# Kernel optimization log

Measured on AMD Instinct MI355X. Metric: run time of the kernel, lower is better.

Reference implementation:

```python
import jax, jax.numpy as jnp
import numpy as np

D_MODEL = 1024
D_STATE = 16
D_CONV = 4
EXPAND = 2
D_INNER = EXPAND * D_MODEL          # 2048
DT_RANK = (D_MODEL + 15) // 16      # 64
BATCH = 1
SEQLEN = 1024


def setup_inputs() -> dict:
    key = jax.random.key(0)
    ks = jax.random.split(key, 9)
    s = 0.02  # weight scale for numerical stability
    x = jax.random.normal(ks[0], (BATCH, SEQLEN, D_MODEL), jnp.float32)
    W_in = jax.random.normal(ks[1], (2 * D_INNER, D_MODEL), jnp.float32) * s
    conv_w = jax.random.normal(ks[2], (D_INNER, D_CONV), jnp.float32) * 0.1
    conv_b = jax.random.normal(ks[3], (D_INNER,), jnp.float32) * 0.1
    W_xproj = jax.random.normal(ks[4], (DT_RANK + 2 * D_STATE, D_INNER), jnp.float32) * s
    W_dt = jax.random.normal(ks[5], (D_INNER, DT_RANK), jnp.float32) * s
    b_dt = jax.random.normal(ks[6], (D_INNER,), jnp.float32) * 0.1
    # official init: A = repeat(arange(1, d_state+1), 'n -> d n'); A_log = log(A)
    A_log = jnp.log(jnp.tile(jnp.arange(1, D_STATE + 1, dtype=jnp.float32), (D_INNER, 1)))
    D_skip = jnp.ones((D_INNER,), jnp.float32)
    W_out = jax.random.normal(ks[7], (D_MODEL, D_INNER), jnp.float32) * s
    return {"x": x, "W_in": W_in, "conv_w": conv_w, "conv_b": conv_b,
            "W_xproj": W_xproj, "W_dt": W_dt, "b_dt": b_dt,
            "A_log": A_log, "D_skip": D_skip, "W_out": W_out}


def _mamba_fwd(x, W_in, conv_w, conv_b, W_xproj, W_dt, b_dt, A_log, D_skip, W_out):
    B, L, _ = x.shape
    # input projection -> (B, L, 2*d_inner), split into x-branch and gate z
    xz = x @ W_in.T
    xi, z = jnp.split(xz, 2, axis=-1)
    # causal depthwise conv1d over length
    xc = jnp.transpose(xi, (0, 2, 1))  # (B, d_inner, L)
    xc = jax.lax.conv_general_dilated(
        xc, conv_w[:, None, :], window_strides=(1,),
        padding=[(D_CONV - 1, 0)], feature_group_count=D_INNER)
    xc = jax.nn.silu(xc + conv_b[None, :, None])
    xi = jnp.transpose(xc, (0, 2, 1))  # (B, L, d_inner)
    # data-dependent SSM parameters
    x_dbl = xi @ W_xproj.T  # (B, L, dt_rank + 2*d_state)
    dt, Bm, Cm = jnp.split(x_dbl, [DT_RANK, DT_RANK + D_STATE], axis=-1)
    delta = jax.nn.softplus(dt @ W_dt.T + b_dt)  # (B, L, d_inner)
    A = -jnp.exp(A_log)  # (d_inner, d_state)
    # discretize: h_t = exp(delta*A) * h_{t-1} + (delta*x) * B_t
    deltaA = jnp.exp(jnp.einsum('bld,dn->bldn', delta, A))          # (B,L,d,n)
    deltaBx = jnp.einsum('bld,bln->bldn', delta * xi, Bm)            # (B,L,d,n)

    def step(h, inp):
        dA_t, dBx_t, c_t = inp
        h = dA_t * h + dBx_t                    # (B, d_inner, d_state)
        y = jnp.einsum('bdn,bn->bd', h, c_t)    # (B, d_inner)
        return h, y

    h0 = jnp.zeros((B, D_INNER, D_STATE), x.dtype)
    _, ys = jax.lax.scan(step, h0, (jnp.transpose(deltaA, (1, 0, 2, 3)),
                                    jnp.transpose(deltaBx, (1, 0, 2, 3)),
                                    jnp.transpose(Cm, (1, 0, 2))))
    y = jnp.transpose(ys, (1, 0, 2))  # (B, L, d_inner)
    y = y + xi * D_skip
    y = y * jax.nn.silu(z)
    return y @ W_out.T  # (B, L, d_model)


def reference(x, W_in, conv_w, conv_b, W_xproj, W_dt, b_dt, A_log, D_skip, W_out):
    return _mamba_fwd(x, W_in, conv_w, conv_b, W_xproj, W_dt, b_dt, A_log, D_skip, W_out)
```

## Files before the change

kernel.cpp:

```cpp
#include <hip/hip_runtime.h>
#include <hip/hip_bf16.h>
#include <math.h>

namespace {

constexpr int SEQ    = 1024;
constexpr int DMODEL = 1024;
constexpr int DINNER = 2048;
constexpr int DSTATE = 16;
constexpr int DTRANK = 64;
constexpr int XPW    = 96;
constexpr int XPWP   = 128;

typedef __attribute__((ext_vector_type(8))) short short8;
typedef __attribute__((ext_vector_type(4))) short short4_t;
typedef __attribute__((ext_vector_type(4))) float floatx4;

#define GLB __attribute__((address_space(1)))
#define LDSAS __attribute__((address_space(3)))

__device__ __forceinline__ float siluf(float x) { return x / (1.f + __expf(-x)); }

__device__ __forceinline__ unsigned short f2b(float f) {
    __hip_bfloat16 h = __float2bfloat16(f);
    return *reinterpret_cast<unsigned short*>(&h);
}
__device__ __forceinline__ float b2f(unsigned short u) {
    union { unsigned int i; float f; } v; v.i = (unsigned int)u << 16; return v.f;
}

constexpr size_t N_XB   = (size_t)SEQ * DMODEL;
constexpr size_t N_WIN  = (size_t)2 * DINNER * DMODEL;
constexpr size_t N_WXP  = (size_t)XPWP * DINNER;
constexpr size_t N_WDT  = (size_t)DINNER * DTRANK;
constexpr size_t N_WOUT = (size_t)DMODEL * DINNER;
constexpr size_t CO1 = N_XB, CO2 = CO1 + N_WIN, CO3 = CO2 + N_WXP,
                 CO4 = CO3 + N_WDT, CO5 = CO4 + N_WOUT;

__global__ __launch_bounds__(256)
void cast_all(const float* __restrict__ x, const float* __restrict__ Win,
              const float* __restrict__ Wxp, const float* __restrict__ Wdt,
              const float* __restrict__ Wout, unsigned short* __restrict__ dst)
{
    size_t i = ((size_t)blockIdx.x * 256 + threadIdx.x) * 8;
    if (i >= CO5) return;
    const float* src; size_t si;
    if (i < CO1)      { src = x;   si = i; }
    else if (i < CO2) { src = Win; si = i - CO1; }
    else if (i < CO3) {
        size_t j = i - CO2, row = j / DINNER;
        if (row >= XPW) { short8 z = {0,0,0,0,0,0,0,0};
                          *reinterpret_cast<short8*>(&dst[i]) = z; return; }
        src = Wxp; si = j;
    }
    else if (i < CO4) { src = Wdt;  si = i - CO3; }
    else              { src = Wout; si = i - CO4; }
    float4 a = *reinterpret_cast<const float4*>(&src[si]);
    float4 b = *reinterpret_cast<const float4*>(&src[si + 4]);
    short8 o;
    o[0]=(short)f2b(a.x); o[1]=(short)f2b(a.y); o[2]=(short)f2b(a.z); o[3]=(short)f2b(a.w);
    o[4]=(short)f2b(b.x); o[5]=(short)f2b(b.y); o[6]=(short)f2b(b.z); o[7]=(short)f2b(b.w);
    *reinterpret_cast<short8*>(&dst[i]) = o;
}

template<int EPI>
__global__ __launch_bounds__(256)
void gemm_mfma(const unsigned short* __restrict__ A, int lda,
               const unsigned short* __restrict__ B, int ldb,
               float* __restrict__ C, int ldc, size_t czstride,
               const float* __restrict__ bias, int Ksub, int nbx)
{
    constexpr int BM = 64, BN = 128, BK = 32, MR = 2, NR = 4;
    __shared__ unsigned short Alds[2][BM * BK];
    __shared__ unsigned short Blds[2][BN * BK];

    const int nwg = gridDim.x;
    int id = blockIdx.x;
    int wg = ((nwg & 7) == 0) ? (id & 7) * (nwg >> 3) + (id >> 3) : id;
    const int bx = wg % nbx, by = wg / nbx;

    const int tid  = threadIdx.x;
    const int lane = tid & 63;
    const int wv   = tid >> 6;
    const int wm   = wv >> 1, wn = wv & 1;
    const int fr   = lane & 15;
    const int kg   = lane >> 4;
    const int m0   = by * BM;
    const int n0   = bx * BN;
    const int kb   = blockIdx.z * Ksub;
    const int srow = tid >> 2;
    const int scol = (tid & 3) * 8;
    float* Cz = C + (size_t)blockIdx.z * czstride;

    floatx4 acc[MR][NR];
#pragma unroll
    for (int mi = 0; mi < MR; ++mi)
#pragma unroll
        for (int ni = 0; ni < NR; ++ni)
            acc[mi][ni] = (floatx4){0.f, 0.f, 0.f, 0.f};

    auto stage = [&](int buf, int k0) {
        __builtin_amdgcn_global_load_lds(
            (const GLB unsigned int*)&A[(size_t)(m0 + srow) * lda + k0 + scol],
            (LDSAS unsigned int*)&Alds[buf][tid * 8], 16, 0, 0);
#pragma unroll
        for (int r = 0; r < 2; ++r)
            __builtin_amdgcn_global_load_lds(
                (const GLB unsigned int*)&B[(size_t)(n0 + r * 64 + srow) * ldb + k0 + scol],
                (LDSAS unsigned int*)&Blds[buf][r * 2048 + tid * 8], 16, 0, 0);
    };

    const int nt = Ksub / BK;
    stage(0, kb);
    __syncthreads();
    int cur = 0;
    for (int t = 0; t < nt; ++t) {
        if (t + 1 < nt) stage(cur ^ 1, kb + (t + 1) * BK);
        short8 af[MR], bf[NR];
#pragma unroll
        for (int mi = 0; mi < MR; ++mi)
            af[mi] = *reinterpret_cast<const short8*>(
                &Alds[cur][(wm * 32 + mi * 16 + fr) * BK + kg * 8]);
#pragma unroll
        for (int ni = 0; ni < NR; ++ni)
            bf[ni] = *reinterpret_cast<const short8*>(
                &Blds[cur][(wn * 64 + ni * 16 + fr) * BK + kg * 8]);
#pragma unroll
        for (int mi = 0; mi < MR; ++mi)
#pragma unroll
            for (int ni = 0; ni < NR; ++ni)
                acc[mi][ni] = __builtin_amdgcn_mfma_f32_16x16x32_bf16(
                    af[mi], bf[ni], acc[mi][ni], 0, 0, 0);
        __syncthreads();
        cur ^= 1;
    }

#pragma unroll
    for (int mi = 0; mi < MR; ++mi)
#pragma unroll
        for (int ni = 0; ni < NR; ++ni)
#pragma unroll
            for (int r = 0; r < 4; ++r) {
                int row = m0 + wm * 32 + mi * 16 + kg * 4 + r;
                int col = n0 + wn * 64 + ni * 16 + fr;
                float v = acc[mi][ni][r];
                if constexpr (EPI == 1) {
                    v += bias[col];
                    v = (v > 20.f) ? v : log1pf(__expf(v));
                }
                Cz[(size_t)row * ldc + col] = v;
            }
}

__global__ __launch_bounds__(256)
void combine_xdbl(const float* __restrict__ xp, float* __restrict__ xf,
                  unsigned short* __restrict__ xb)
{
    int i = (blockIdx.x * 256 + threadIdx.x) * 4;
    constexpr size_t SL = (size_t)SEQ * XPWP;
    float4 s{0.f, 0.f, 0.f, 0.f};
#pragma unroll
    for (int z = 0; z < 8; ++z) {
        float4 p = *reinterpret_cast<const float4*>(&xp[z * SL + i]);
        s.x += p.x; s.y += p.y; s.z += p.z; s.w += p.w;
    }
    *reinterpret_cast<float4*>(&xf[i]) = s;
    short4_t o; o[0]=(short)f2b(s.x); o[1]=(short)f2b(s.y);
                o[2]=(short)f2b(s.z); o[3]=(short)f2b(s.w);
    *reinterpret_cast<short4_t*>(&xb[i]) = o;
}

__global__ __launch_bounds__(256)
void combine_out(const float* __restrict__ op, float* __restrict__ out)
{
    int i = (blockIdx.x * 256 + threadIdx.x) * 4;
    constexpr size_t SL = (size_t)SEQ * DMODEL;
    float4 s0 = *reinterpret_cast<const float4*>(&op[i]);
    float4 s1 = *reinterpret_cast<const float4*>(&op[SL + i]);
    float4 s2 = *reinterpret_cast<const float4*>(&op[2 * SL + i]);
    float4 s3 = *reinterpret_cast<const float4*>(&op[3 * SL + i]);
    float4 s{ s0.x+s1.x+s2.x+s3.x, s0.y+s1.y+s2.y+s3.y,
              s0.z+s1.z+s2.z+s3.z, s0.w+s1.w+s2.w+s3.w };
    *reinterpret_cast<float4*>(&out[i]) = s;
}

__global__ __launch_bounds__(256)
void conv_silu(const float* __restrict__ xz,
               const float* __restrict__ conv_w,
               const float* __restrict__ conv_b,
               unsigned short* __restrict__ xic)
{
    int idx = blockIdx.x * 256 + threadIdx.x;
    int l = idx / DINNER;
    int d = idx % DINNER;
    float acc = conv_b[d];
    float4 w = *reinterpret_cast<const float4*>(&conv_w[d * 4]);
    float wk[4] = {w.x, w.y, w.z, w.w};
#pragma unroll
    for (int k = 0; k < 4; ++k) {
        int ls = l - 3 + k;
        if (ls >= 0) acc = fmaf(xz[(size_t)ls * (2 * DINNER) + d], wk[k], acc);
    }
    xic[idx] = f2b(siluf(acc));
}

__global__ __launch_bounds__(256)
void scan_pass1(const float* __restrict__ delta,
                const unsigned short* __restrict__ xic,
                const float* __restrict__ xdbl,
                const float* __restrict__ A_log,
                float* __restrict__ Pbuf, float* __restrict__ Sbuf, int CH)
{
    const int tid = threadIdx.x;
    const int d   = blockIdx.x * 256 + tid;
    const int c   = blockIdx.y;
    const int tb  = c * CH;

    float An[16], h[16];
#pragma unroll
    for (int n = 0; n < 16; ++n) {
        An[n] = -__expf(A_log[(size_t)d * 16 + n]);
        h[n]  = 0.f;
    }
    float sdl = 0.f;

    __shared__ float Bls[16][16];
    const int sr = tid >> 4, sq = tid & 15;

    for (int s0 = 0; s0 < CH; s0 += 16) {
        Bls[sr][sq] = xdbl[(size_t)(tb + s0 + sr) * XPWP + DTRANK + sq];
        __syncthreads();
#pragma unroll
        for (int tt = 0; tt < 16; ++tt) {
            int t = tb + s0 + tt;
            float dl = delta[(size_t)t * DINNER + d];
            float xv = b2f(xic[(size_t)t * DINNER + d]);
            float t1 = dl * xv;
            sdl += dl;
            floatx4 B0 = *reinterpret_cast<const floatx4*>(&Bls[tt][0]);
            floatx4 B1 = *reinterpret_cast<const floatx4*>(&Bls[tt][4]);
            floatx4 B2 = *reinterpret_cast<const floatx4*>(&Bls[tt][8]);
            floatx4 B3 = *reinterpret_cast<const floatx4*>(&Bls[tt][12]);
#pragma unroll
            for (int n = 0; n < 16; ++n) {
                float bn = (n < 4) ? B0[n] : (n < 8) ? B1[n-4] : (n < 12) ? B2[n-8] : B3[n-12];
                float a  = __expf(dl * An[n]);
                h[n] = fmaf(a, h[n], t1 * bn);
            }
        }
        __syncthreads();
    }
#pragma unroll
    for (int n = 0; n < 16; ++n) {
        size_t o = ((size_t)c * 16 + n) * DINNER + d;
        Pbuf[o] = __expf(sdl * An[n]);
        Sbuf[o] = h[n];
    }
}

__global__ __launch_bounds__(256)
void scan_pass2(const float* __restrict__ Pbuf, float* __restrict__ Sbuf, int NCr)
{
    int idx = blockIdx.x * 256 + threadIdx.x;
    float h = 0.f;
    for (int c = 0; c < NCr; ++c) {
        size_t o = (size_t)c * (DINNER * DSTATE) + idx;
        float p = Pbuf[o], s = Sbuf[o];
        Sbuf[o] = h;
        h = fmaf(p, h, s);
    }
}

__global__ __launch_bounds__(256)
void scan_pass3(const float* __restrict__ delta,
                const unsigned short* __restrict__ xic,
                const float* __restrict__ xdbl,
                const float* __restrict__ A_log,
                const float* __restrict__ D_skip,
                const float* __restrict__ xz,
                const float* __restrict__ Hin,
                unsigned short* __restrict__ yfin, int CH)
{
    const int tid = threadIdx.x;
    const int d   = blockIdx.x * 256 + tid;
    const int c   = blockIdx.y;
    const int tb  = c * CH;

    float An[16], h[16];
#pragma unroll
    for (int n = 0; n < 16; ++n) {
        An[n] = -__expf(A_log[(size_t)d * 16 + n]);
        h[n]  = Hin[((size_t)c * 16 + n) * DINNER + d];
    }
    const float Dsk = D_skip[d];

    __shared__ float Bls[16][32];
    const int sr = tid >> 4, sq = (tid & 15) * 2;

    for (int s0 = 0; s0 < CH; s0 += 16) {
        float2 bc = *reinterpret_cast<const float2*>(
            &xdbl[(size_t)(tb + s0 + sr) * XPWP + DTRANK + sq]);
        Bls[sr][sq] = bc.x; Bls[sr][sq + 1] = bc.y;
        __syncthreads();
#pragma unroll
        for (int tt = 0; tt < 16; ++tt) {
            int t = tb + s0 + tt;
            float dl = delta[(size_t)t * DINNER + d];
            float xv = b2f(xic[(size_t)t * DINNER + d]);
            float zv = xz[(size_t)t * (2 * DINNER) + DINNER + d];
            float t1 = dl * xv;
            floatx4 B0 = *reinterpret_cast<const floatx4*>(&Bls[tt][0]);
            floatx4 B1 = *reinterpret_cast<const floatx4*>(&Bls[tt][4]);
            floatx4 B2 = *reinterpret_cast<const floatx4*>(&Bls[tt][8]);
            floatx4 B3 = *reinterpret_cast<const floatx4*>(&Bls[tt][12]);
            floatx4 C0 = *reinterpret_cast<const floatx4*>(&Bls[tt][16]);
            floatx4 C1 = *reinterpret_cast<const floatx4*>(&Bls[tt][20]);
            floatx4 C2 = *reinterpret_cast<const floatx4*>(&Bls[tt][24]);
            floatx4 C3 = *reinterpret_cast<const floatx4*>(&Bls[tt][28]);
            float y = 0.f;
#pragma unroll
            for (int n = 0; n < 16; ++n) {
                float bn = (n < 4) ? B0[n] : (n < 8) ? B1[n-4] : (n < 12) ? B2[n-8] : B3[n-12];
                float cn = (n < 4) ? C0[n] : (n < 8) ? C1[n-4] : (n < 12) ? C2[n-8] : C3[n-12];
                float a  = __expf(dl * An[n]);
                h[n] = fmaf(a, h[n], t1 * bn);
                y = fmaf(h[n], cn, y);
            }
            float yv = fmaf(xv, Dsk, y) * siluf(zv);
            yfin[(size_t)t * DINNER + d] = f2b(yv);
        }
        __syncthreads();
    }
}

}

extern "C" void kernel_launch(void* const* d_in, const int* in_sizes, int n_in,
                              void* d_out, int out_size, void* d_ws, size_t ws_size,
                              hipStream_t stream)
{
    (void)in_sizes; (void)n_in; (void)out_size;

    const float* x       = (const float*)d_in[0];
    const float* W_in    = (const float*)d_in[1];
    const float* conv_w  = (const float*)d_in[2];
    const float* conv_b  = (const float*)d_in[3];
    const float* W_xproj = (const float*)d_in[4];
    const float* W_dt    = (const float*)d_in[5];
    const float* b_dt    = (const float*)d_in[6];
    const float* A_log   = (const float*)d_in[7];
    const float* D_skip  = (const float*)d_in[8];
    const float* W_out   = (const float*)d_in[9];
    float* out = (float*)d_out;

    const size_t BF16_SHORTS = CO5 + (size_t)SEQ * DINNER + (size_t)SEQ * XPWP
                             + (size_t)SEQ * DINNER;
    const size_t F32_FIXED   = (size_t)SEQ * 2 * DINNER
                             + (size_t)SEQ * DINNER
                             + (size_t)SEQ * XPWP
                             + 8 * (size_t)SEQ * XPWP;
    auto need = [&](int nc) {
        return (F32_FIXED + 2 * (size_t)nc * DINNER * DSTATE) * 4 + BF16_SHORTS * 2;
    };
    int NC = 64;
    if (need(64) > ws_size) NC = 32;
    if (need(32) > ws_size) NC = 16;
    const int CH = SEQ / NC;

    float* ws     = (float*)d_ws;
    float* xz     = ws;
    float* delta  = xz    + (size_t)SEQ * 2 * DINNER;
    float* xdbl_f = delta + (size_t)SEQ * DINNER;
    float* xpart  = xdbl_f + (size_t)SEQ * XPWP;
    float* Pbuf   = xpart + 8 * (size_t)SEQ * XPWP;
    float* Sbuf   = Pbuf  + (size_t)NC * DINNER * DSTATE;
    unsigned short* us     = (unsigned short*)(Sbuf + (size_t)NC * DINNER * DSTATE);
    unsigned short* x_b    = us;
    unsigned short* Win_b  = x_b + CO1;
    unsigned short* Wxp_b  = x_b + CO2;
    unsigned short* Wdt_b  = x_b + CO3;
    unsigned short* Wout_b = x_b + CO4;
    unsigned short* xic_b  = x_b + CO5;
    unsigned short* xdbl_b = xic_b + (size_t)SEQ * DINNER;
    unsigned short* yfin_b = xdbl_b + (size_t)SEQ * XPWP;
    float* opart = xz;

    cast_all<<<(int)((CO5 / 8 + 255) / 256), 256, 0, stream>>>(
        x, W_in, W_xproj, W_dt, W_out, x_b);

    gemm_mfma<0><<<dim3(512, 1, 1), 256, 0, stream>>>(
        x_b, DMODEL, Win_b, DMODEL, xz, 2 * DINNER, 0, nullptr, DMODEL, 32);

    conv_silu<<<(SEQ * DINNER) / 256, 256, 0, stream>>>(xz, conv_w, conv_b, xic_b);

    gemm_mfma<0><<<dim3(16, 1, 8), 256, 0, stream>>>(
        xic_b, DINNER, Wxp_b, DINNER, xpart, XPWP, (size_t)SEQ * XPWP,
        nullptr, DINNER / 8, 1);
    combine_xdbl<<<(SEQ * XPWP) / 1024, 256, 0, stream>>>(xpart, xdbl_f, xdbl_b);

    gemm_mfma<1><<<dim3(256, 1, 1), 256, 0, stream>>>(
        xdbl_b, XPWP, Wdt_b, DTRANK, delta, DINNER, 0, b_dt, DTRANK, 16);

    scan_pass1<<<dim3(DINNER / 256, NC), 256, 0, stream>>>(
        delta, xic_b, xdbl_f, A_log, Pbuf, Sbuf, CH);
    scan_pass2<<<(DINNER * DSTATE) / 256, 256, 0, stream>>>(Pbuf, Sbuf, NC);
    scan_pass3<<<dim3(DINNER / 256, NC), 256, 0, stream>>>(
        delta, xic_b, xdbl_f, A_log, D_skip, xz, Sbuf, yfin_b, CH);

    gemm_mfma<0><<<dim3(128, 1, 4), 256, 0, stream>>>(
        yfin_b, DINNER, Wout_b, DINNER, opart, DMODEL, (size_t)SEQ * DMODEL,
        nullptr, DINNER / 4, 8);
    combine_out<<<(SEQ * DMODEL) / 1024, 256, 0, stream>>>(opart, out);
}
```

Baseline: 136.7 us.

## Shrink GEMM tile to 64x64, fuse silu(z) bf16 epilogue, halve out-proj split-K

Reduces the GEMM tile from 64x128 to 64x64 and doubles grid sizes for all projections. The input-projection epilogue now writes the x-branch in fp32 and the gate as bf16 silu(z), which removes the fp32 z buffer and the silu from the scan. The output projection drops from 4-way to 2-way split-K, so the combine step reads less. Smaller tiles give more workgroups but less data reuse per block, and storing the gate in bf16 adds a little rounding error.

```diff
diff --git a/kernel.cpp b/kernel.cpp
--- a/kernel.cpp
+++ b/kernel.cpp
@@ -68,9 +68,10 @@
 void gemm_mfma(const unsigned short* __restrict__ A, int lda,
                const unsigned short* __restrict__ B, int ldb,
                float* __restrict__ C, int ldc, size_t czstride,
-               const float* __restrict__ bias, int Ksub, int nbx)
-{
-    constexpr int BM = 64, BN = 128, BK = 32, MR = 2, NR = 4;
+               const float* __restrict__ bias, int Ksub, int nbx,
+               unsigned short* __restrict__ gz)
+{
+    constexpr int BM = 64, BN = 64, BK = 32, MR = 2, NR = 2;
     __shared__ unsigned short Alds[2][BM * BK];
     __shared__ unsigned short Blds[2][BN * BK];
 
@@ -103,11 +104,9 @@
         __builtin_amdgcn_global_load_lds(
             (const GLB unsigned int*)&A[(size_t)(m0 + srow) * lda + k0 + scol],
             (LDSAS unsigned int*)&Alds[buf][tid * 8], 16, 0, 0);
-#pragma unroll
-        for (int r = 0; r < 2; ++r)
-            __builtin_amdgcn_global_load_lds(
-                (const GLB unsigned int*)&B[(size_t)(n0 + r * 64 + srow) * ldb + k0 + scol],
-                (LDSAS unsigned int*)&Blds[buf][r * 2048 + tid * 8], 16, 0, 0);
+        __builtin_amdgcn_global_load_lds(
+            (const GLB unsigned int*)&B[(size_t)(n0 + srow) * ldb + k0 + scol],
+            (LDSAS unsigned int*)&Blds[buf][tid * 8], 16, 0, 0);
     };
 
     const int nt = Ksub / BK;
@@ -124,7 +123,7 @@
 #pragma unroll
         for (int ni = 0; ni < NR; ++ni)
             bf[ni] = *reinterpret_cast<const short8*>(
-                &Blds[cur][(wn * 64 + ni * 16 + fr) * BK + kg * 8]);
+                &Blds[cur][(wn * 32 + ni * 16 + fr) * BK + kg * 8]);
 #pragma unroll
         for (int mi = 0; mi < MR; ++mi)
 #pragma unroll
@@ -142,13 +141,20 @@
 #pragma unroll
             for (int r = 0; r < 4; ++r) {
                 int row = m0 + wm * 32 + mi * 16 + kg * 4 + r;
-                int col = n0 + wn * 64 + ni * 16 + fr;
+                int col = n0 + wn * 32 + ni * 16 + fr;
                 float v = acc[mi][ni][r];
                 if constexpr (EPI == 1) {
                     v += bias[col];
                     v = (v > 20.f) ? v : log1pf(__expf(v));
+                    Cz[(size_t)row * ldc + col] = v;
+                } else if constexpr (EPI == 3) {
+                    if (col < DINNER)
+                        Cz[(size_t)row * ldc + col] = v;
+                    else
+                        gz[(size_t)row * DINNER + col - DINNER] = f2b(siluf(v));
+                } else {
+                    Cz[(size_t)row * ldc + col] = v;
                 }
-                Cz[(size_t)row * ldc + col] = v;
             }
 }
 
@@ -177,15 +183,12 @@
     constexpr size_t SL = (size_t)SEQ * DMODEL;
     float4 s0 = *reinterpret_cast<const float4*>(&op[i]);
     float4 s1 = *reinterpret_cast<const float4*>(&op[SL + i]);
-    float4 s2 = *reinterpret_cast<const float4*>(&op[2 * SL + i]);
-    float4 s3 = *reinterpret_cast<const float4*>(&op[3 * SL + i]);
-    float4 s{ s0.x+s1.x+s2.x+s3.x, s0.y+s1.y+s2.y+s3.y,
-              s0.z+s1.z+s2.z+s3.z, s0.w+s1.w+s2.w+s3.w };
+    float4 s{ s0.x+s1.x, s0.y+s1.y, s0.z+s1.z, s0.w+s1.w };
     *reinterpret_cast<float4*>(&out[i]) = s;
 }
 
 __global__ __launch_bounds__(256)
-void conv_silu(const float* __restrict__ xz,
+void conv_silu(const float* __restrict__ xi,
                const float* __restrict__ conv_w,
                const float* __restrict__ conv_b,
                unsigned short* __restrict__ xic)
@@ -199,7 +202,7 @@
 #pragma unroll
     for (int k = 0; k < 4; ++k) {
         int ls = l - 3 + k;
-        if (ls >= 0) acc = fmaf(xz[(size_t)ls * (2 * DINNER) + d], wk[k], acc);
+        if (ls >= 0) acc = fmaf(xi[(size_t)ls * DINNER + d], wk[k], acc);
     }
     xic[idx] = f2b(siluf(acc));
 }
@@ -277,7 +280,7 @@
                 const float* __restrict__ xdbl,
                 const float* __restrict__ A_log,
                 const float* __restrict__ D_skip,
-                const float* __restrict__ xz,
+                const unsigned short* __restrict__ gz,
                 const float* __restrict__ Hin,
                 unsigned short* __restrict__ yfin, int CH)
 {
@@ -307,7 +310,7 @@
             int t = tb + s0 + tt;
             float dl = delta[(size_t)t * DINNER + d];
             float xv = b2f(xic[(size_t)t * DINNER + d]);
-            float zv = xz[(size_t)t * (2 * DINNER) + DINNER + d];
+            float zv = b2f(gz[(size_t)t * DINNER + d]);
             float t1 = dl * xv;
             floatx4 B0 = *reinterpret_cast<const floatx4*>(&Bls[tt][0]);
             floatx4 B1 = *reinterpret_cast<const floatx4*>(&Bls[tt][4]);
@@ -326,7 +329,7 @@
                 h[n] = fmaf(a, h[n], t1 * bn);
                 y = fmaf(h[n], cn, y);
             }
-            float yv = fmaf(xv, Dsk, y) * siluf(zv);
+            float yv = fmaf(xv, Dsk, y) * zv;
             yfin[(size_t)t * DINNER + d] = f2b(yv);
         }
         __syncthreads();
@@ -353,10 +356,8 @@
     const float* W_out   = (const float*)d_in[9];
     float* out = (float*)d_out;
 
-    const size_t BF16_SHORTS = CO5 + (size_t)SEQ * DINNER + (size_t)SEQ * XPWP
-                             + (size_t)SEQ * DINNER;
-    const size_t F32_FIXED   = (size_t)SEQ * 2 * DINNER
-                             + (size_t)SEQ * DINNER
+    const size_t BF16_SHORTS = CO5 + 3 * (size_t)SEQ * DINNER + (size_t)SEQ * XPWP;
+    const size_t F32_FIXED   = 2 * (size_t)SEQ * DINNER
                              + (size_t)SEQ * XPWP
                              + 8 * (size_t)SEQ * XPWP;
     auto need = [&](int nc) {
@@ -368,8 +369,8 @@
     const int CH = SEQ / NC;
 
     float* ws     = (float*)d_ws;
-    float* xz     = ws;
-    float* delta  = xz    + (size_t)SEQ * 2 * DINNER;
+    float* xi_f   = ws;
+    float* delta  = xi_f  + (size_t)SEQ * DINNER;
     float* xdbl_f = delta + (size_t)SEQ * DINNER;
     float* xpart  = xdbl_f + (size_t)SEQ * XPWP;
     float* Pbuf   = xpart + 8 * (size_t)SEQ * XPWP;
@@ -383,32 +384,33 @@
     unsigned short* xic_b  = x_b + CO5;
     unsigned short* xdbl_b = xic_b + (size_t)SEQ * DINNER;
     unsigned short* yfin_b = xdbl_b + (size_t)SEQ * XPWP;
-    float* opart = xz;
+    unsigned short* gz_b   = yfin_b + (size_t)SEQ * DINNER;
+    float* opart = xi_f;
 
     cast_all<<<(int)((CO5 / 8 + 255) / 256), 256, 0, stream>>>(
         x, W_in, W_xproj, W_dt, W_out, x_b);
 
-    gemm_mfma<0><<<dim3(512, 1, 1), 256, 0, stream>>>(
-        x_b, DMODEL, Win_b, DMODEL, xz, 2 * DINNER, 0, nullptr, DMODEL, 32);
-
-    conv_silu<<<(SEQ * DINNER) / 256, 256, 0, stream>>>(xz, conv_w, conv_b, xic_b);
-
-    gemm_mfma<0><<<dim3(16, 1, 8), 256, 0, stream>>>(
+    gemm_mfma<3><<<dim3(1024, 1, 1), 256, 0, stream>>>(
+        x_b, DMODEL, Win_b, DMODEL, xi_f, DINNER, 0, nullptr, DMODEL, 64, gz_b);
+
+    conv_silu<<<(SEQ * DINNER) / 256, 256, 0, stream>>>(xi_f, conv_w, conv_b, xic_b);
+
+    gemm_mfma<0><<<dim3(32, 1, 8), 256, 0, stream>>>(
         xic_b, DINNER, Wxp_b, DINNER, xpart, XPWP, (size_t)SEQ * XPWP,
-        nullptr, DINNER / 8, 1);
+        nullptr, DINNER / 8, 2, nullptr);
     combine_xdbl<<<(SEQ * XPWP) / 1024, 256, 0, stream>>>(xpart, xdbl_f, xdbl_b);
 
-    gemm_mfma<1><<<dim3(256, 1, 1), 256, 0, stream>>>(
-        xdbl_b, XPWP, Wdt_b, DTRANK, delta, DINNER, 0, b_dt, DTRANK, 16);
+    gemm_mfma<1><<<dim3(512, 1, 1), 256, 0, stream>>>(
+        xdbl_b, XPWP, Wdt_b, DTRANK, delta, DINNER, 0, b_dt, DTRANK, 32, nullptr);
 
     scan_pass1<<<dim3(DINNER / 256, NC), 256, 0, stream>>>(
         delta, xic_b, xdbl_f, A_log, Pbuf, Sbuf, CH);
     scan_pass2<<<(DINNER * DSTATE) / 256, 256, 0, stream>>>(Pbuf, Sbuf, NC);
     scan_pass3<<<dim3(DINNER / 256, NC), 256, 0, stream>>>(
-        delta, xic_b, xdbl_f, A_log, D_skip, xz, Sbuf, yfin_b, CH);
-
-    gemm_mfma<0><<<dim3(128, 1, 4), 256, 0, stream>>>(
+        delta, xic_b, xdbl_f, A_log, D_skip, gz_b, Sbuf, yfin_b, CH);
+
+    gemm_mfma<0><<<dim3(256, 1, 2), 256, 0, stream>>>(
         yfin_b, DINNER, Wout_b, DINNER, opart, DMODEL, (size_t)SEQ * DMODEL,
-        nullptr, DINNER / 4, 8);
+        nullptr, DINNER / 2, 16, nullptr);
     combine_out<<<(SEQ * DMODEL) / 1024, 256, 0, stream>>>(opart, out);
 }
```

Result: slower. 143.3 us (+4.8%).
